# Kernel optimization log

Measured on AMD Instinct MI355X. Metric: run time of the kernel, lower is better.

The kernel has to match this reference:

```python
import jax, jax.numpy as jnp
import numpy as np

B, S, EMBED, HEADS = 2, 2048, 1024, 16
HEAD = EMBED // HEADS


def setup_inputs() -> dict:
    key = jax.random.key(0)
    ks = jax.random.split(key, 8)
    inp = {
        "values": jax.random.normal(ks[0], (B, S, EMBED), jnp.float32),
        "keys": jax.random.normal(ks[1], (B, S, EMBED), jnp.float32),
        "queries": jax.random.normal(ks[2], (B, S, EMBED), jnp.float32),
        # causal mask, broadcast over batch and heads; masked_fill where mask==0
        "mask": jnp.tril(jnp.ones((S, S), jnp.bool_))[None, None, :, :],
        # torch nn.Linear weights: y = x @ W.T (+ b)
        "Wv": jax.random.normal(ks[3], (HEAD, HEAD), jnp.float32) / np.sqrt(HEAD),
        "Wk": jax.random.normal(ks[4], (HEAD, HEAD), jnp.float32) / np.sqrt(HEAD),
        "Wq": jax.random.normal(ks[5], (HEAD, HEAD), jnp.float32) / np.sqrt(HEAD),
        "Wo": jax.random.normal(ks[6], (EMBED, EMBED), jnp.float32) / np.sqrt(EMBED),
        "bo": jax.random.normal(ks[7], (EMBED,), jnp.float32) * 0.01,
    }
    return inp


def reference(values, keys, queries, mask, Wv, Wk, Wq, Wo, bo):
    N, Lq = queries.shape[0], queries.shape[1]
    Lk = keys.shape[1]
    # split heads: [B, L, H, D]
    v = values.reshape(N, -1, HEADS, HEAD) @ Wv.T
    k = keys.reshape(N, Lk, HEADS, HEAD) @ Wk.T
    q = queries.reshape(N, Lq, HEADS, HEAD) @ Wq.T
    # scores [B, H, Lq, Lk]
    energy = jnp.einsum('bqhd,bkhd->bhqk', q, k)
    energy = jnp.where(mask, energy, jnp.float32(-1e20))
    attn = jax.nn.softmax(energy / np.sqrt(HEAD), axis=-1)
    out = jnp.einsum('bhqk,bkhd->bqhd', attn, v).reshape(N, Lq, EMBED)
    return out @ Wo.T + bo
```

## Files before the change

kernel.cpp:

```cpp
#include <hip/hip_runtime.h>
#include <hip/hip_bf16.h>
#include <math.h>

constexpr int Bc = 2;
constexpr int Sc = 2048;
constexpr int E  = 1024;
constexpr int Hn = 16;
constexpr int Dh = 64;

typedef short bf16x8 __attribute__((ext_vector_type(8)));
typedef float f32x4  __attribute__((ext_vector_type(4)));

#define MFMA16(a, b, c) __builtin_amdgcn_mfma_f32_16x16x32_bf16((a), (b), (c), 0, 0, 0)

constexpr float QSCALE = 0.125f * 1.4426950408889634f;
constexpr float FIXED_M2 = 18.0f;

__device__ inline bf16x8 load8(const __hip_bfloat16* p) {
    return *reinterpret_cast<const bf16x8*>(p);
}

__device__ inline unsigned short f2b(float x) {
    __hip_bfloat16 h = __float2bfloat16(x);
    unsigned short u;
    __builtin_memcpy(&u, &h, 2);
    return u;
}

__device__ inline ushort4 pack4(float a, float b, float c, float d) {
    __hip_bfloat162 lo = __float22bfloat162_rn(make_float2(a, b));
    __hip_bfloat162 hi = __float22bfloat162_rn(make_float2(c, d));
    ushort4 u;
    __builtin_memcpy(&u.x, &lo, 4);
    __builtin_memcpy(&u.z, &hi, 4);
    return u;
}

__device__ inline bf16x8 cvt8(const float* p) {
    float4 a = *reinterpret_cast<const float4*>(p);
    float4 b = *reinterpret_cast<const float4*>(p + 4);
    ushort4 lo = pack4(a.x, a.y, a.z, a.w);
    ushort4 hi = pack4(b.x, b.y, b.z, b.w);
    bf16x8 r;
    __builtin_memcpy(&r, &lo, 8);
    __builtin_memcpy(reinterpret_cast<char*>(&r) + 8, &hi, 8);
    return r;
}

__device__ inline float fast_exp2(float x) {
#if __has_builtin(__builtin_amdgcn_exp2f)
    return __builtin_amdgcn_exp2f(x);
#else
    return exp2f(x);
#endif
}


__global__ __launch_bounds__(256) void cvt_w(
    const float* __restrict__ Wo, const float* __restrict__ Wq,
    const float* __restrict__ Wk, const float* __restrict__ Wv,
    __hip_bfloat16* __restrict__ Wf, __hip_bfloat16* __restrict__ Wf3) {
    const int i = blockIdx.x * 256 + threadIdx.x;
    if (i < 131072) {
        const int l16 = i & 15, quad = (i >> 4) & 3;
        const int kk = (i >> 6) & 31, ct = i >> 11;
        bf16x8 v = cvt8(Wo + (size_t)(ct * 16 + l16) * E + kk * 32 + quad * 8);
        *reinterpret_cast<bf16x8*>(Wf + (size_t)i * 8) = v;
    } else {
        const int idx = i - 131072;
        const int m = idx >> 9, r = idx & 511;
        const int lane = r & 63, nh = r >> 6;
        const int nt = nh >> 1, half = nh & 1;
        const int quad = lane >> 4, l16 = lane & 15;
        const float* Wm = (m == 0) ? Wq : (m == 1) ? Wk : Wv;
        bf16x8 v = cvt8(Wm + (nt * 16 + l16) * 64 + half * 32 + quad * 8);
        *reinterpret_cast<bf16x8*>(Wf3 + (size_t)idx * 8) = v;
    }
}

__global__ __launch_bounds__(256) void qkv_proj(
    const float* __restrict__ vals,
    const float* __restrict__ keys,
    const float* __restrict__ quer,
    const __hip_bfloat16* __restrict__ Wf3,
    __hip_bfloat16* __restrict__ Qf,
    __hip_bfloat16* __restrict__ Kf,
    __hip_bfloat16* __restrict__ Vf)
{
    __shared__ __align__(16) __hip_bfloat16 X[3][64 * 72];

    const int bid = blockIdx.x;
    const int st  = bid & 31;
    const int h   = (bid >> 5) & 15;
    const int b   = bid >> 9;
    const int sbase = st * 64;
    const int tid = threadIdx.x;

    const float* srcs[3] = { quer, keys, vals };
#pragma unroll
    for (int m = 0; m < 3; ++m) {
        for (int i = tid; i < 512; i += 256) {
            const int r = i >> 3, c = i & 7;
            bf16x8 v = cvt8(srcs[m] + (size_t)(b * Sc + sbase + r) * E + h * 64 + c * 8);
            *reinterpret_cast<bf16x8*>(&X[m][r * 72 + c * 8]) = v;
        }
    }
    __syncthreads();

    const int lane = tid & 63, w = tid >> 6;
    const int quad = lane >> 4, l16 = lane & 15;
    const int bh = b * Hn + h;
    const size_t bhoff = (size_t)bh * 131072;

#pragma unroll
    for (int m = 0; m < 2; ++m) {
        bf16x8 xb0 = load8(&X[m][(w * 16 + l16) * 72 + quad * 8]);
        bf16x8 xb1 = load8(&X[m][(w * 16 + l16) * 72 + quad * 8 + 32]);
#pragma unroll
        for (int ntd = 0; ntd < 4; ++ntd) {
            bf16x8 wa0 = load8(Wf3 + ((size_t)(m * 8 + ntd * 2 + 0) * 64 + lane) * 8);
            bf16x8 wa1 = load8(Wf3 + ((size_t)(m * 8 + ntd * 2 + 1) * 64 + lane) * 8);
            f32x4 acc = (f32x4){0.f, 0.f, 0.f, 0.f};
            acc = MFMA16(wa0, xb0, acc);
            acc = MFMA16(wa1, xb1, acc);
            const int half   = ntd >> 1;
            const int quad_f = (ntd & 1) * 2 + (quad >> 1);
            const int j0     = (quad & 1) * 4;
            if (m == 0) {
                const int t = st * 4 + w;
                *reinterpret_cast<ushort4*>(
                    Qf + bhoff + ((size_t)(t * 2 + half) * 64 + quad_f * 16 + l16) * 8 + j0) =
                    pack4(acc[0] * QSCALE, acc[1] * QSCALE, acc[2] * QSCALE, acc[3] * QSCALE);
            } else {
                *reinterpret_cast<ushort4*>(
                    Kf + bhoff + (((size_t)(st * 4 + w) * 2 + half) * 64 + quad_f * 16 + l16) * 8 + j0) =
                    pack4(acc[0], acc[1], acc[2], acc[3]);
            }
        }
    }

    {
        bf16x8 xa0 = load8(&X[2][(w * 16 + l16) * 72 + quad * 8]);
        bf16x8 xa1 = load8(&X[2][(w * 16 + l16) * 72 + quad * 8 + 32]);
        const int half   = w >> 1;
        const int quad_f = (w & 1) * 2 + (quad >> 1);
        const int j0     = (quad & 1) * 4;
#pragma unroll
        for (int nt = 0; nt < 4; ++nt) {
            bf16x8 wb0 = load8(Wf3 + ((size_t)(16 + nt * 2 + 0) * 64 + lane) * 8);
            bf16x8 wb1 = load8(Wf3 + ((size_t)(16 + nt * 2 + 1) * 64 + lane) * 8);
            f32x4 acc = (f32x4){0.f, 0.f, 0.f, 0.f};
            acc = MFMA16(xa0, wb0, acc);
            acc = MFMA16(xa1, wb1, acc);
            *reinterpret_cast<ushort4*>(
                Vf + bhoff + (((size_t)(st * 4 + nt) * 2 + half) * 64 + quad_f * 16 + l16) * 8 + j0) =
                pack4(acc[0], acc[1], acc[2], acc[3]);
        }
    }
}

__global__ __launch_bounds__(128, 2) void flash_attn(
    const __hip_bfloat16* __restrict__ Qf,
    const __hip_bfloat16* __restrict__ Kf,
    const __hip_bfloat16* __restrict__ Vf,
    __hip_bfloat16* __restrict__ Af)
{
    __shared__ __align__(16) __hip_bfloat16 P[2][2][16 * 72];
    __shared__ __align__(16) float OB[4][16 * 68];
    __shared__ float LB[4][16];

    const int bid = blockIdx.x;
    const int bh = bid & 31;
    const int u  = 31 - (bid >> 5);
    const int h  = bh & 15;
    const int b  = bh >> 4;
    const int tid = threadIdx.x, lane = tid & 63, hf = tid >> 6;
    const int quad = lane >> 4, l16 = lane & 15;
    const int nk = u + 1;

    const __hip_bfloat16* Qp = Qf + (size_t)bh * 131072;
    const __hip_bfloat16* Kp = Kf + (size_t)bh * 131072;
    const __hip_bfloat16* Vp = Vf + (size_t)bh * 131072;

    bf16x8 onesf;
#pragma unroll
    for (int q = 0; q < 8; ++q) onesf[q] = (short)0x3F80;

    bf16x8 qa[4], qb[4];
#pragma unroll
    for (int i = 0; i < 4; ++i) {
        qa[i] = load8(Qp + ((size_t)((4 * u + i) * 2 + 0) * 64 + lane) * 8);
        qb[i] = load8(Qp + ((size_t)((4 * u + i) * 2 + 1) * 64 + lane) * 8);
    }

    f32x4 oa[4][4];
    f32x4 ls[4];
#pragma unroll
    for (int i = 0; i < 4; ++i) {
        ls[i] = (f32x4){0.f, 0.f, 0.f, 0.f};
#pragma unroll
        for (int nt = 0; nt < 4; ++nt) oa[i][nt] = (f32x4){0.f, 0.f, 0.f, 0.f};
    }

    bf16x8 ka[4], kb[4];
#pragma unroll
    for (int nt = 0; nt < 4; ++nt) {
        const size_t o = (((size_t)hf * 4 + nt) * 2) * 512;
        ka[nt] = load8(Kp + o + lane * 8);
        kb[nt] = load8(Kp + o + 512 + lane * 8);
    }

    bf16x8 va[4], vb[4];

    for (int kt = hf; kt < nk; kt += 2) {
#pragma unroll
        for (int nt = 0; nt < 4; ++nt) {
            const size_t o = (((size_t)kt * 4 + nt) * 2) * 512;
            va[nt] = load8(Vp + o + lane * 8);
            vb[nt] = load8(Vp + o + 512 + lane * 8);
        }

        const int kbase = kt * 64;
        const bool diag = (kt == nk - 1);

        auto scores = [&](int i, int s) {
            f32x4 sc[4];
#pragma unroll
            for (int ntk = 0; ntk < 4; ++ntk) {
                f32x4 z = (f32x4){-FIXED_M2, -FIXED_M2, -FIXED_M2, -FIXED_M2};
                z = MFMA16(ka[ntk], qa[i], z);
                z = MFMA16(kb[ntk], qb[i], z);
                sc[ntk] = z;
            }
            if (diag) {
                const int qrow = (4 * u + i) * 16 + l16;
#pragma unroll
                for (int ntk = 0; ntk < 4; ++ntk)
#pragma unroll
                    for (int r = 0; r < 4; ++r)
                        if (kbase + ntk * 16 + quad * 4 + r > qrow) sc[ntk][r] = -1e30f;
            }
#pragma unroll
            for (int ntk = 0; ntk < 4; ++ntk) {
                *reinterpret_cast<ushort4*>(&P[hf][s][l16 * 72 + ntk * 16 + quad * 4]) =
                    pack4(fast_exp2(sc[ntk][0]), fast_exp2(sc[ntk][1]),
                          fast_exp2(sc[ntk][2]), fast_exp2(sc[ntk][3]));
            }
        };
        auto pv = [&](int i, int s) {
            bf16x8 pf0 = load8(&P[hf][s][l16 * 72 + quad * 8]);
            bf16x8 pf1 = load8(&P[hf][s][l16 * 72 + quad * 8 + 32]);
#pragma unroll
            for (int nt = 0; nt < 4; ++nt) {
                oa[i][nt] = MFMA16(va[nt], pf0, oa[i][nt]);
                oa[i][nt] = MFMA16(vb[nt], pf1, oa[i][nt]);
            }
            ls[i] = MFMA16(onesf, pf0, ls[i]);
            ls[i] = MFMA16(onesf, pf1, ls[i]);
        };

        scores(0, 0);
        scores(1, 1);
        pv(0, 0);
        pv(1, 1);
        scores(2, 0);
        scores(3, 1);

        {
            const int nkt = (kt + 2 < nk) ? kt + 2 : kt;
#pragma unroll
            for (int nt = 0; nt < 4; ++nt) {
                const size_t o = (((size_t)nkt * 4 + nt) * 2) * 512;
                ka[nt] = load8(Kp + o + lane * 8);
                kb[nt] = load8(Kp + o + 512 + lane * 8);
            }
        }

        pv(2, 0);
        pv(3, 1);
    }

    if (hf == 1) {
#pragma unroll
        for (int i = 0; i < 4; ++i) {
#pragma unroll
            for (int nt = 0; nt < 4; ++nt)
                *reinterpret_cast<float4*>(&OB[i][l16 * 68 + nt * 16 + quad * 4]) =
                    (float4){ oa[i][nt][0], oa[i][nt][1], oa[i][nt][2], oa[i][nt][3] };
            if (quad == 0) LB[i][l16] = ls[i][0];
        }
    }
    __syncthreads();
    if (hf == 0) {
#pragma unroll
        for (int i = 0; i < 4; ++i) {
            const float inv = 1.0f / (ls[i][0] + LB[i][l16]);
            const int rt = b * 128 + 4 * u + i;
#pragma unroll
            for (int nt = 0; nt < 4; ++nt) {
                float4 ob = *reinterpret_cast<float4*>(&OB[i][l16 * 68 + nt * 16 + quad * 4]);
                const int kk     = h * 2 + (nt >> 1);
                const int quad_f = (nt & 1) * 2 + (quad >> 1);
                const int j0     = (quad & 1) * 4;
                *reinterpret_cast<ushort4*>(
                    Af + (((size_t)rt * 32 + kk) * 64 + quad_f * 16 + l16) * 8 + j0) =
                    pack4((oa[i][nt][0] + ob.x) * inv, (oa[i][nt][1] + ob.y) * inv,
                          (oa[i][nt][2] + ob.z) * inv, (oa[i][nt][3] + ob.w) * inv);
            }
        }
    }
}

__global__ __launch_bounds__(256) void out_proj(
    const __hip_bfloat16* __restrict__ Af,
    const __hip_bfloat16* __restrict__ Wf,
    const float* __restrict__ bo,
    float* __restrict__ out)
{
    const int bid = blockIdx.x;
    const int cb = bid & 15;
    const int rb = bid >> 4;
    const int tid = threadIdx.x, lane = tid & 63, w = tid >> 6;
    const int quad = lane >> 4, l16 = lane & 15;
    const int rt0 = rb * 8 + w;
    const int cbase = cb * 64;

    const __hip_bfloat16* pa0 = Af + ((size_t)rt0 * 32) * 512 + lane * 8;
    const __hip_bfloat16* pa1 = pa0 + 4 * 32 * 512;
    const __hip_bfloat16* pw  = Wf + ((size_t)cb * 4 * 32) * 512 + lane * 8;

    f32x4 acc[2][4];
#pragma unroll
    for (int u = 0; u < 2; ++u)
#pragma unroll
        for (int nt = 0; nt < 4; ++nt) acc[u][nt] = (f32x4){0.f, 0.f, 0.f, 0.f};

    bf16x8 af0[2], af1[2], bf[4][2];
#pragma unroll
    for (int s = 0; s < 2; ++s) {
        const size_t ko = (size_t)s * 512;
        af0[s] = load8(pa0 + ko);
        af1[s] = load8(pa1 + ko);
#pragma unroll
        for (int nt = 0; nt < 4; ++nt) bf[nt][s] = load8(pw + (size_t)nt * 32 * 512 + ko);
    }

    for (int kk = 0; kk < 32; kk += 2) {
#pragma unroll
        for (int s = 0; s < 2; ++s) {
            const int kn = kk + 2 + s;
            const size_t ko = (size_t)((kn < 32) ? kn : kk + s) * 512;
            bf16x8 naf0 = load8(pa0 + ko), naf1 = load8(pa1 + ko);
            bf16x8 nbf[4];
#pragma unroll
            for (int nt = 0; nt < 4; ++nt) nbf[nt] = load8(pw + (size_t)nt * 32 * 512 + ko);
#pragma unroll
            for (int nt = 0; nt < 4; ++nt) {
                acc[0][nt] = MFMA16(af0[s], bf[nt][s], acc[0][nt]);
                acc[1][nt] = MFMA16(af1[s], bf[nt][s], acc[1][nt]);
            }
            af0[s] = naf0; af1[s] = naf1;
#pragma unroll
            for (int nt = 0; nt < 4; ++nt) bf[nt][s] = nbf[nt];
        }
    }
#pragma unroll
    for (int nt = 0; nt < 4; ++nt) {
        const float bv = bo[cbase + nt * 16 + l16];
#pragma unroll
        for (int u = 0; u < 2; ++u)
#pragma unroll
            for (int r = 0; r < 4; ++r) {
                const int row = (rt0 + u * 4) * 16 + quad * 4 + r;
                out[(size_t)row * E + cbase + nt * 16 + l16] = acc[u][nt][r] + bv;
            }
    }
}

extern "C" void kernel_launch(void* const* d_in, const int* in_sizes, int n_in,
                              void* d_out, int out_size, void* d_ws, size_t ws_size,
                              hipStream_t stream) {
    const float* vals = (const float*)d_in[0];
    const float* keys = (const float*)d_in[1];
    const float* quer = (const float*)d_in[2];
    const float* Wv = (const float*)d_in[4];
    const float* Wk = (const float*)d_in[5];
    const float* Wq = (const float*)d_in[6];
    const float* Wo = (const float*)d_in[7];
    const float* bo = (const float*)d_in[8];
    float* out = (float*)d_out;

    __hip_bfloat16* ws = (__hip_bfloat16*)d_ws;
    constexpr size_t NTOK = (size_t)Bc * Hn * Sc * Dh;
    __hip_bfloat16* Qw  = ws;
    __hip_bfloat16* Kw  = ws + NTOK;
    __hip_bfloat16* Vw  = ws + 2 * NTOK;
    __hip_bfloat16* Aw  = ws + 3 * NTOK;
    __hip_bfloat16* Wof = ws + 4 * NTOK;
    __hip_bfloat16* Wf3 = Wof + (size_t)E * E;

    hipLaunchKernelGGL(cvt_w, dim3(518), dim3(256), 0, stream, Wo, Wq, Wk, Wv, Wof, Wf3);
    hipLaunchKernelGGL(qkv_proj, dim3(Bc * Hn * (Sc / 64)), dim3(256), 0, stream,
                       vals, keys, quer, Wf3, Qw, Kw, Vw);
    hipLaunchKernelGGL(flash_attn, dim3(32 * 32), dim3(128), 0, stream,
                       Qw, Kw, Vw, Aw);
    hipLaunchKernelGGL(out_proj, dim3(32 * 16), dim3(256), 0, stream,
                       Aw, Wof, bo, out);
}
```

Before: 171.4 us.

## Reorder flash-attention loop to compute all scores before PV and serpentine block order

The P shared buffer grows from two slots to four per wave, so the four score tiles are computed back-to-back before any PV MFMAs. The K reload then sits between the two phases. This is meant to give the scheduler longer runs of independent MFMA and exp work and more latency hiding. The block-to-query-tile mapping also changes from descending order to a serpentine order within groups of eight, to rebalance causal work across concurrently resident blocks. The cost is extra LDS use, which may affect occupancy.

```diff
diff --git a/kernel.cpp b/kernel.cpp
--- a/kernel.cpp
+++ b/kernel.cpp
@@ -165,13 +165,15 @@
     const __hip_bfloat16* __restrict__ Vf,
     __hip_bfloat16* __restrict__ Af)
 {
-    __shared__ __align__(16) __hip_bfloat16 P[2][2][16 * 72];
+    __shared__ __align__(16) __hip_bfloat16 P[2][4][16 * 72];
     __shared__ __align__(16) float OB[4][16 * 68];
     __shared__ float LB[4][16];
 
     const int bid = blockIdx.x;
     const int bh = bid & 31;
-    const int u  = 31 - (bid >> 5);
+    const int ip = bid >> 5;
+    const int qg = ip >> 3, rg = ip & 7;
+    const int u  = 8 * qg + ((qg & 1) ? (7 - rg) : rg);
     const int h  = bh & 15;
     const int b  = bh >> 4;
     const int tid = threadIdx.x, lane = tid & 63, hf = tid >> 6;
@@ -223,7 +225,7 @@
         const int kbase = kt * 64;
         const bool diag = (kt == nk - 1);
 
-        auto scores = [&](int i, int s) {
+        auto scores = [&](int i) {
             f32x4 sc[4];
 #pragma unroll
             for (int ntk = 0; ntk < 4; ++ntk) {
@@ -242,14 +244,14 @@
             }
 #pragma unroll
             for (int ntk = 0; ntk < 4; ++ntk) {
-                *reinterpret_cast<ushort4*>(&P[hf][s][l16 * 72 + ntk * 16 + quad * 4]) =
+                *reinterpret_cast<ushort4*>(&P[hf][i][l16 * 72 + ntk * 16 + quad * 4]) =
                     pack4(fast_exp2(sc[ntk][0]), fast_exp2(sc[ntk][1]),
                           fast_exp2(sc[ntk][2]), fast_exp2(sc[ntk][3]));
             }
         };
-        auto pv = [&](int i, int s) {
-            bf16x8 pf0 = load8(&P[hf][s][l16 * 72 + quad * 8]);
-            bf16x8 pf1 = load8(&P[hf][s][l16 * 72 + quad * 8 + 32]);
+        auto pv = [&](int i) {
+            bf16x8 pf0 = load8(&P[hf][i][l16 * 72 + quad * 8]);
+            bf16x8 pf1 = load8(&P[hf][i][l16 * 72 + quad * 8 + 32]);
 #pragma unroll
             for (int nt = 0; nt < 4; ++nt) {
                 oa[i][nt] = MFMA16(va[nt], pf0, oa[i][nt]);
@@ -259,12 +261,10 @@
             ls[i] = MFMA16(onesf, pf1, ls[i]);
         };
 
-        scores(0, 0);
-        scores(1, 1);
-        pv(0, 0);
-        pv(1, 1);
-        scores(2, 0);
-        scores(3, 1);
+        scores(0);
+        scores(1);
+        scores(2);
+        scores(3);
 
         {
             const int nkt = (kt + 2 < nk) ? kt + 2 : kt;
@@ -276,8 +276,10 @@
             }
         }
 
-        pv(2, 0);
-        pv(3, 1);
+        pv(0);
+        pv(1);
+        pv(2);
+        pv(3);
     }
 
     if (hf == 1) {
```

Result: no change. 168.6 us (-1.7%).
